# Kernel tuning notes

Measured on AMD Instinct MI355X. Metric: run time of the kernel, lower is better.

The kernel has to match this reference:

```python
import jax, jax.numpy as jnp
import numpy as np

N, D, H, E = 8192, 1024, 4096, 8


def setup_inputs() -> dict:
    key = jax.random.key(0)
    ks = jax.random.split(key, 7)
    s_d = 1.0 / np.sqrt(D)
    s_h = 1.0 / np.sqrt(H)
    return {
        "x": jax.random.normal(ks[0], (N, D), dtype=jnp.float32),
        "gate_w": jax.random.uniform(ks[1], (E, D), jnp.float32, -s_d, s_d),
        "gate_b": jax.random.uniform(ks[2], (E,), jnp.float32, -s_d, s_d),
        "w1": jax.random.uniform(ks[3], (E, D, H), jnp.float32, -s_d, s_d),
        "b1": jax.random.uniform(ks[4], (E, H), jnp.float32, -s_d, s_d),
        "w2": jax.random.uniform(ks[5], (E, H, D), jnp.float32, -s_h, s_h),
        "b2": jax.random.uniform(ks[6], (E, D), jnp.float32, -s_h, s_h),
    }


def reference(x, gate_w, gate_b, w1, b1, w2, b2):
    # gate softmax over experts: [N, E]
    gates = jax.nn.softmax(x @ gate_w.T + gate_b, axis=-1)
    # all experts in one batched GEMM pair
    h = jax.nn.relu(jnp.einsum("nd,edh->neh", x, w1) + b1)      # [N, E, H]
    expert_out = jnp.einsum("neh,ehd->ned", h, w2) + b2          # [N, E, D]
    # gated weighted sum over experts
    return jnp.einsum("ne,ned->nd", gates, expert_out)
```

## Files before the change

### kernel.cpp

```cpp
#include <hip/hip_runtime.h>
#include <hip/hip_bf16.h>

typedef _Float16 half8 __attribute__((ext_vector_type(8)));
typedef float floatx4 __attribute__((ext_vector_type(4)));

__device__ inline void gload_lds16(const void* g, void* l) {
  __builtin_amdgcn_global_load_lds(
      (const __attribute__((address_space(1))) unsigned int*)g,
      (__attribute__((address_space(3))) unsigned int*)l, 16, 0, 0);
}

__device__ inline unsigned lds_off(const void* p) {
  return (unsigned)(uintptr_t)(const __attribute__((address_space(3))) char*)p;
}
__device__ inline half8 ds_read128(unsigned off) {
  half8 r;
  asm volatile("ds_read_b128 %0, %1" : "=v"(r) : "v"(off));
  return r;
}

#define BARB()   __builtin_amdgcn_s_barrier()
#define WAITL0() asm volatile("s_waitcnt lgkmcnt(0)")
#define WAITV(n) asm volatile("s_waitcnt vmcnt(" #n ")")
#define SCHED0() __builtin_amdgcn_sched_barrier(0)

__device__ inline void xcd_chunk_decode(int* mb, int* nk) {
  const int gx = gridDim.x;
  const int nb = gx * gridDim.y;
  const int b = blockIdx.x + gx * blockIdx.y;
  const int s = (b & 7) * (nb >> 3) + (b >> 3);
  const int PW = gx * 8;
  const int p = s / PW, r = s % PW;
  *mb = r >> 3;
  *nk = p * 8 + (r & 7);
}

__global__ __launch_bounds__(256) void gates_kernel(
    const float* __restrict__ x, const float* __restrict__ gw,
    const float* __restrict__ gb, float* __restrict__ gates) {
  const int lane = threadIdx.x & 63, wid = threadIdx.x >> 6;
  const int n = blockIdx.x * 4 + wid;
  const float* xr = x + (size_t)n * 1024;
  float xv[16];
#pragma unroll
  for (int i = 0; i < 16; ++i) xv[i] = xr[lane + i * 64];
  float logit[8];
#pragma unroll
  for (int e = 0; e < 8; ++e) {
    const float* wr = gw + (size_t)e * 1024;
    float p = 0.f;
#pragma unroll
    for (int i = 0; i < 16; ++i) p += xv[i] * wr[lane + i * 64];
#pragma unroll
    for (int off = 32; off > 0; off >>= 1) p += __shfl_xor(p, off);
    logit[e] = p + gb[e];
  }
  float mx = logit[0];
#pragma unroll
  for (int e = 1; e < 8; ++e) mx = fmaxf(mx, logit[e]);
  float s = 0.f;
#pragma unroll
  for (int e = 0; e < 8; ++e) { logit[e] = expf(logit[e] - mx); s += logit[e]; }
  if (lane < 8) gates[(size_t)n * 8 + lane] = logit[lane] / s;
}

__global__ __launch_bounds__(256) void bias_init_kernel(
    const float* __restrict__ gates, const float* __restrict__ b2,
    float* __restrict__ out) {
  const int idx = blockIdx.x * 256 + threadIdx.x;
  const int n = idx >> 8;
  const int d = (idx & 255) << 2;
  const float* g = gates + (size_t)n * 8;
  floatx4 acc = {0.f, 0.f, 0.f, 0.f};
#pragma unroll
  for (int e = 0; e < 8; ++e) {
    const float ge = g[e];
    const floatx4 b = *(const floatx4*)(b2 + (size_t)e * 1024 + d);
#pragma unroll
    for (int j = 0; j < 4; ++j) acc[j] += ge * b[j];
  }
  *(floatx4*)(out + (size_t)n * 1024 + d) = acc;
}

__global__ __launch_bounds__(256) void cvt_f32_f16_kernel(
    const float* __restrict__ in, _Float16* __restrict__ out, int n8) {
  const int i = blockIdx.x * 256 + threadIdx.x;
  if (i >= n8) return;
  const float4* p = (const float4*)(in + (size_t)i * 8);
  float4 a = p[0], b = p[1];
  half8 h;
  h[0] = (_Float16)a.x; h[1] = (_Float16)a.y; h[2] = (_Float16)a.z; h[3] = (_Float16)a.w;
  h[4] = (_Float16)b.x; h[5] = (_Float16)b.y; h[6] = (_Float16)b.z; h[7] = (_Float16)b.w;
  *(half8*)(out + (size_t)i * 8) = h;
}

__global__ __launch_bounds__(256) void transpose_cvt_kernel(
    const float* __restrict__ in, _Float16* __restrict__ out, int R, int C) {
  __shared__ _Float16 tile[32][33];
  const float* src = in + (size_t)blockIdx.z * R * C;
  _Float16* dst = out + (size_t)blockIdx.z * R * C;
  const int tx = threadIdx.x & 31, ty = threadIdx.x >> 5;
  const int c0 = blockIdx.x << 5, r0 = blockIdx.y << 5;
#pragma unroll
  for (int i = 0; i < 4; ++i)
    tile[ty + i * 8][tx] = (_Float16)src[(size_t)(r0 + ty + i * 8) * C + c0 + tx];
  __syncthreads();
#pragma unroll
  for (int i = 0; i < 4; ++i)
    dst[(size_t)(c0 + ty + i * 8) * R + r0 + tx] = tile[tx][ty + i * 8];
}

__global__ __launch_bounds__(512, 2) void gemm1_kernel(
    const _Float16* __restrict__ A, const _Float16* __restrict__ Bt,
    const float* __restrict__ bias, const float* __restrict__ gates, int e,
    _Float16* __restrict__ Hout, int lda, int ldb, int K, int Nout) {
  __shared__ _Float16 smem[2][4][8192];
  const int tid = threadIdx.x, lane = tid & 63, wid = tid >> 6;
  const int wm = wid >> 2, wn = wid & 3;

  int mb, nk;
  xcd_chunk_decode(&mb, &nk);
  const int m0 = mb * 256, n0 = nk * 256;
  const int NT = K >> 6;

  floatx4 acc[8][4] = {};

  auto stage_half = [&](int h) {
    if (h >= 4 * NT) return;
    const int th = h >> 2, j = h & 3, bf = th & 1;
    const int k0 = th * 64;
    const char* gb; int ld, rorig;
    if (j < 2) { gb = (const char*)A;  ld = lda; rorig = m0 + j * 128; }
    else       { gb = (const char*)Bt; ld = ldb; rorig = n0 + (j - 2) * 128; }
    _Float16* lb = &smem[bf][j][0];
#pragma unroll
    for (int i = 0; i < 2; ++i) {
      const int row = (wid * 2 + i) * 8 + (lane >> 3);
      const int gkb = ((lane & 7) * 16) ^ ((row & 7) << 4);
      gload_lds16(gb + ((size_t)(rorig + row) * ld + k0) * 2 + gkb,
                  lb + (wid * 2 + i) * 512 + lane * 8);
    }
  };

  const unsigned smem0 = lds_off(&smem[0][0][0]);
  auto ldA = [&](int bf, int mf, int ks) -> half8 {
    const int row = mf * 16 + (lane & 15);
    const int col = (ks * 64 + ((lane >> 4) << 4)) ^ ((row & 7) << 4);
    return ds_read128(smem0 + (bf * 4 + wm) * 16384 + row * 128 + col);
  };
  auto ldB = [&](int bf, int nf, int ks) -> half8 {
    const int c = wn * 64 + nf * 16 + (lane & 15);
    const int r = c & 127;
    const int col = (ks * 64 + ((lane >> 4) << 4)) ^ ((r & 7) << 4);
    return ds_read128(smem0 + (bf * 4 + 2 + (c >> 7)) * 16384 + r * 128 + col);
  };

  stage_half(0); stage_half(1); stage_half(2); stage_half(3);
  stage_half(4 * 1 + 2); stage_half(4 * 1 + 3);
  WAITV(4); SCHED0();
  BARB();

#pragma unroll 1
  for (int t = 0; t < NT; ++t) {
    const int bf = t & 1;
    half8 a[4][2], bh[2][2], bl[2][2];
#pragma unroll
    for (int ks = 0; ks < 2; ++ks) {
#pragma unroll
      for (int m = 0; m < 4; ++m) a[m][ks] = ldA(bf, m, ks);
#pragma unroll
      for (int n = 0; n < 2; ++n) bh[n][ks] = ldB(bf, 2 + n, ks);
    }
    stage_half(4 * (t + 1) + 0);
    BARB(); WAITL0(); SCHED0();
    __builtin_amdgcn_s_setprio(1);
#pragma unroll
    for (int m = 0; m < 4; ++m)
#pragma unroll
      for (int n = 0; n < 2; ++n)
#pragma unroll
        for (int ks = 0; ks < 2; ++ks)
          acc[m][2 + n] = __builtin_amdgcn_mfma_f32_16x16x32_f16(
              a[m][ks], bh[n][ks], acc[m][2 + n], 0, 0, 0);
    __builtin_amdgcn_s_setprio(0);
    BARB();
#pragma unroll
    for (int ks = 0; ks < 2; ++ks)
#pragma unroll
      for (int n = 0; n < 2; ++n) bl[n][ks] = ldB(bf, n, ks);
    stage_half(4 * (t + 1) + 1);
    BARB(); WAITL0(); SCHED0();
    __builtin_amdgcn_s_setprio(1);
#pragma unroll
    for (int m = 0; m < 4; ++m)
#pragma unroll
      for (int n = 0; n < 2; ++n)
#pragma unroll
        for (int ks = 0; ks < 2; ++ks)
          acc[m][n] = __builtin_amdgcn_mfma_f32_16x16x32_f16(
              a[m][ks], bl[n][ks], acc[m][n], 0, 0, 0);
    __builtin_amdgcn_s_setprio(0);
    BARB();
#pragma unroll
    for (int ks = 0; ks < 2; ++ks)
#pragma unroll
      for (int m = 0; m < 4; ++m) a[m][ks] = ldA(bf, 4 + m, ks);
    stage_half(4 * (t + 2) + 2);
    BARB(); WAITL0(); SCHED0();
    __builtin_amdgcn_s_setprio(1);
#pragma unroll
    for (int m = 0; m < 4; ++m)
#pragma unroll
      for (int n = 0; n < 2; ++n)
#pragma unroll
        for (int ks = 0; ks < 2; ++ks)
          acc[4 + m][2 + n] = __builtin_amdgcn_mfma_f32_16x16x32_f16(
              a[m][ks], bh[n][ks], acc[4 + m][2 + n], 0, 0, 0);
    __builtin_amdgcn_s_setprio(0);
    BARB();
    stage_half(4 * (t + 2) + 3);
    BARB();
    __builtin_amdgcn_s_setprio(1);
#pragma unroll
    for (int m = 0; m < 4; ++m)
#pragma unroll
      for (int n = 0; n < 2; ++n)
#pragma unroll
        for (int ks = 0; ks < 2; ++ks)
          acc[4 + m][n] = __builtin_amdgcn_mfma_f32_16x16x32_f16(
              a[m][ks], bl[n][ks], acc[4 + m][n], 0, 0, 0);
    __builtin_amdgcn_s_setprio(0);
    if (t + 2 < NT) { WAITV(4); } else { WAITV(0); }
    SCHED0();
    BARB();
  }

#pragma unroll
  for (int mf = 0; mf < 8; ++mf) {
    const int gr0 = m0 + wm * 128 + mf * 16 + ((lane >> 4) << 2);
#pragma unroll
    for (int r = 0; r < 4; ++r) {
      const float g = gates[(size_t)(gr0 + r) * 8 + e];
#pragma unroll
      for (int nf = 0; nf < 4; ++nf) {
        const int gc = n0 + wn * 64 + nf * 16 + (lane & 15);
        const float v = acc[mf][nf][r] + bias[gc];
        Hout[(size_t)(gr0 + r) * Nout + gc] = (_Float16)(g * fmaxf(v, 0.0f));
      }
    }
  }
}

__global__ __launch_bounds__(512, 2) void gemm2_kernel(
    const _Float16* __restrict__ A, const _Float16* __restrict__ Bt,
    float* __restrict__ Out, int lda, int ldb, int K, int Nout) {
  __shared__ _Float16 smem[3][3][8192];
  const int tid = threadIdx.x, lane = tid & 63, wid = tid >> 6;
  const int wm = wid >> 2, wn = wid & 3;

  int mb, nk;
  xcd_chunk_decode(&mb, &nk);
  const int m0 = mb * 256, n0 = nk * 128;
  const int NT = K >> 6;

  floatx4 acc[8][2] = {};

  auto stage_half = [&](int tile, int j) {
    if (tile >= NT) return;
    const int bf = tile % 3;
    const int k0 = tile * 64;
    const char* gb; int ld, rorig;
    if (j < 2) { gb = (const char*)A;  ld = lda; rorig = m0 + j * 128; }
    else       { gb = (const char*)Bt; ld = ldb; rorig = n0; }
    _Float16* lb = &smem[bf][j][0];
#pragma unroll
    for (int i = 0; i < 2; ++i) {
      const int row = (wid * 2 + i) * 8 + (lane >> 3);
      const int gkb = ((lane & 7) * 16) ^ ((row & 7) << 4);
      gload_lds16(gb + ((size_t)(rorig + row) * ld + k0) * 2 + gkb,
                  lb + (wid * 2 + i) * 512 + lane * 8);
    }
  };

  const unsigned smem0 = lds_off(&smem[0][0][0]);
  auto ldA = [&](int bf, int mf, int ks) -> half8 {
    const int row = mf * 16 + (lane & 15);
    const int col = (ks * 64 + ((lane >> 4) << 4)) ^ ((row & 7) << 4);
    return ds_read128(smem0 + (bf * 3 + wm) * 16384 + row * 128 + col);
  };
  auto ldB = [&](int bf, int nf, int ks) -> half8 {
    const int r = wn * 32 + nf * 16 + (lane & 15);
    const int col = (ks * 64 + ((lane >> 4) << 4)) ^ ((r & 7) << 4);
    return ds_read128(smem0 + (bf * 3 + 2) * 16384 + r * 128 + col);
  };

  stage_half(0, 0); stage_half(0, 1); stage_half(0, 2);
  stage_half(1, 0); stage_half(1, 1); stage_half(1, 2);
  WAITV(6); SCHED0();
  BARB();

#pragma unroll 1
  for (int t = 0; t < NT; ++t) {
    const int bf = t % 3;
    half8 a[4][2], bb[2][2];
#pragma unroll
    for (int ks = 0; ks < 2; ++ks) {
#pragma unroll
      for (int m = 0; m < 4; ++m) a[m][ks] = ldA(bf, m, ks);
#pragma unroll
      for (int n = 0; n < 2; ++n) bb[n][ks] = ldB(bf, n, ks);
    }
    stage_half(t + 2, 0); stage_half(t + 2, 1);
    BARB(); WAITL0(); SCHED0();
    __builtin_amdgcn_s_setprio(1);
#pragma unroll
    for (int m = 0; m < 4; ++m)
#pragma unroll
      for (int n = 0; n < 2; ++n)
#pragma unroll
        for (int ks = 0; ks < 2; ++ks)
          acc[m][n] = __builtin_amdgcn_mfma_f32_16x16x32_f16(
              a[m][ks], bb[n][ks], acc[m][n], 0, 0, 0);
    __builtin_amdgcn_s_setprio(0);
    BARB();
#pragma unroll
    for (int ks = 0; ks < 2; ++ks)
#pragma unroll
      for (int m = 0; m < 4; ++m) a[m][ks] = ldA(bf, 4 + m, ks);
    stage_half(t + 2, 2);
    BARB(); WAITL0(); SCHED0();
    __builtin_amdgcn_s_setprio(1);
#pragma unroll
    for (int m = 0; m < 4; ++m)
#pragma unroll
      for (int n = 0; n < 2; ++n)
#pragma unroll
        for (int ks = 0; ks < 2; ++ks)
          acc[4 + m][n] = __builtin_amdgcn_mfma_f32_16x16x32_f16(
              a[m][ks], bb[n][ks], acc[4 + m][n], 0, 0, 0);
    __builtin_amdgcn_s_setprio(0);
    if (t + 2 < NT) { WAITV(6); } else { WAITV(0); }
    SCHED0();
    BARB();
  }

#pragma unroll
  for (int mf = 0; mf < 8; ++mf) {
    const int gr0 = m0 + wm * 128 + mf * 16 + ((lane >> 4) << 2);
#pragma unroll
    for (int nf = 0; nf < 2; ++nf) {
      const int gc = n0 + wn * 32 + nf * 16 + (lane & 15);
#pragma unroll
      for (int r = 0; r < 4; ++r) {
        float* p = Out + (size_t)(gr0 + r) * Nout + gc;
        *p = *p + acc[mf][nf][r];
      }
    }
  }
}

extern "C" void kernel_launch(void* const* d_in, const int* in_sizes, int n_in,
                              void* d_out, int out_size, void* d_ws,
                              size_t ws_size, hipStream_t stream) {
  const float* x  = (const float*)d_in[0];
  const float* gw = (const float*)d_in[1];
  const float* gb = (const float*)d_in[2];
  const float* w1 = (const float*)d_in[3];
  const float* b1 = (const float*)d_in[4];
  const float* w2 = (const float*)d_in[5];
  const float* b2 = (const float*)d_in[6];
  float* out = (float*)d_out;

  const int N = 8192, D = 1024, H = 4096, E = 8;
  const size_t MB = 1ull << 20;

  char* ws = (char*)d_ws;
  float* gates  = (float*)ws;
  _Float16* x_h = (_Float16*)(ws + MB);

  gates_kernel<<<N / 4, 256, 0, stream>>>(x, gw, gb, gates);
  bias_init_kernel<<<N * D / 4 / 256, 256, 0, stream>>>(gates, b2, out);
  cvt_f32_f16_kernel<<<(N * D / 8 + 255) / 256, 256, 0, stream>>>(x, x_h, N * D / 8);

  if (ws_size >= 210 * MB) {
    _Float16* Hbuf = (_Float16*)(ws + 17 * MB);
    _Float16* w1t  = (_Float16*)(ws + 81 * MB);
    _Float16* w2t  = (_Float16*)(ws + 145 * MB);
    transpose_cvt_kernel<<<dim3(H / 32, D / 32, E), 256, 0, stream>>>(w1, w1t, D, H);
    transpose_cvt_kernel<<<dim3(D / 32, H / 32, E), 256, 0, stream>>>(w2, w2t, H, D);
    for (int e = 0; e < E; ++e) {
      gemm1_kernel<<<dim3(N / 256, H / 256), 512, 0, stream>>>(
          x_h, w1t + (size_t)e * H * D, b1 + (size_t)e * H, gates, e, Hbuf,
          D, D, D, H);
      gemm2_kernel<<<dim3(N / 256, D / 128), 512, 0, stream>>>(
          Hbuf, w2t + (size_t)e * D * H, out, H, H, H, D);
    }
  } else {
    _Float16* w1t  = (_Float16*)(ws + 17 * MB);
    _Float16* w2t  = (_Float16*)(ws + 25 * MB);
    _Float16* Hbuf = (_Float16*)(ws + 33 * MB);
    for (int e = 0; e < E; ++e) {
      transpose_cvt_kernel<<<dim3(H / 32, D / 32, 1), 256, 0, stream>>>(
          w1 + (size_t)e * D * H, w1t, D, H);
      transpose_cvt_kernel<<<dim3(D / 32, H / 32, 1), 256, 0, stream>>>(
          w2 + (size_t)e * H * D, w2t, H, D);
      gemm1_kernel<<<dim3(N / 256, H / 256), 512, 0, stream>>>(
          x_h, w1t, b1 + (size_t)e * H, gates, e, Hbuf, D, D, D, H);
      gemm2_kernel<<<dim3(N / 256, D / 128), 512, 0, stream>>>(
          Hbuf, w2t, out, H, H, H, D);
    }
  }
}
```

Measured before the change: 1.379 ms.

## Use 256x256 split-K tile for second GEMM with separate partial buffers

The second GEMM now reuses the 256x256-tile kernel template in place of the 256x128 one. K is split in two halves, and each half accumulates into its own fp32 buffer (partial or out), so the two halves never write the same location. A final combine kernel adds the partials and the gated b2 bias, replacing the up-front bias init. The w1 transpose now runs per expert into a small buffer, which lowers the workspace requirement but puts a transpose kernel inside the loop.

```diff
diff --git a/kernel.cpp b/kernel.cpp
--- a/kernel.cpp
+++ b/kernel.cpp
@@ -9,7 +9,6 @@
       (const __attribute__((address_space(1))) unsigned int*)g,
       (__attribute__((address_space(3))) unsigned int*)l, 16, 0, 0);
 }
-
 __device__ inline unsigned lds_off(const void* p) {
   return (unsigned)(uintptr_t)(const __attribute__((address_space(3))) char*)p;
 }
@@ -18,7 +17,6 @@
   asm volatile("ds_read_b128 %0, %1" : "=v"(r) : "v"(off));
   return r;
 }
-
 #define BARB()   __builtin_amdgcn_s_barrier()
 #define WAITL0() asm volatile("s_waitcnt lgkmcnt(0)")
 #define WAITV(n) asm volatile("s_waitcnt vmcnt(" #n ")")
@@ -72,6 +70,27 @@
   const int d = (idx & 255) << 2;
   const float* g = gates + (size_t)n * 8;
   floatx4 acc = {0.f, 0.f, 0.f, 0.f};
+#pragma unroll
+  for (int e = 0; e < 8; ++e) {
+    const float ge = g[e];
+    const floatx4 b = *(const floatx4*)(b2 + (size_t)e * 1024 + d);
+#pragma unroll
+    for (int j = 0; j < 4; ++j) acc[j] += ge * b[j];
+  }
+  *(floatx4*)(out + (size_t)n * 1024 + d) = acc;
+}
+
+__global__ __launch_bounds__(256) void combine_kernel(
+    const float* __restrict__ gates, const float* __restrict__ b2,
+    const float* __restrict__ partial, float* __restrict__ out) {
+  const int idx = blockIdx.x * 256 + threadIdx.x;
+  const int n = idx >> 8;
+  const int d = (idx & 255) << 2;
+  const float* g = gates + (size_t)n * 8;
+  floatx4 acc = *(const floatx4*)(partial + (size_t)n * 1024 + d);
+  const floatx4 o = *(const floatx4*)(out + (size_t)n * 1024 + d);
+#pragma unroll
+  for (int j = 0; j < 4; ++j) acc[j] += o[j];
 #pragma unroll
   for (int e = 0; e < 8; ++e) {
     const float ge = g[e];
@@ -110,25 +129,30 @@
     dst[(size_t)(c0 + ty + i * 8) * R + r0 + tx] = tile[tx][ty + i * 8];
 }
 
-__global__ __launch_bounds__(512, 2) void gemm1_kernel(
+template <int EPI>
+__global__ __launch_bounds__(512, 2) void gemm256_kernel(
     const _Float16* __restrict__ A, const _Float16* __restrict__ Bt,
     const float* __restrict__ bias, const float* __restrict__ gates, int e,
-    _Float16* __restrict__ Hout, int lda, int ldb, int K, int Nout) {
+    _Float16* __restrict__ Hout, float* __restrict__ partial,
+    float* __restrict__ outp, int beta, int lda, int ldb, int kLen, int Nout) {
   __shared__ _Float16 smem[2][4][8192];
   const int tid = threadIdx.x, lane = tid & 63, wid = tid >> 6;
   const int wm = wid >> 2, wn = wid & 3;
 
   int mb, nk;
   xcd_chunk_decode(&mb, &nk);
-  const int m0 = mb * 256, n0 = nk * 256;
-  const int NT = K >> 6;
+  const int m0 = mb * 256;
+  int n0, kb;
+  if (EPI == 1) { n0 = (nk & 3) * 256; kb = (nk >> 2) * kLen; }
+  else          { n0 = nk * 256;       kb = 0; }
+  const int NT = kLen >> 6;
 
   floatx4 acc[8][4] = {};
 
   auto stage_half = [&](int h) {
     if (h >= 4 * NT) return;
     const int th = h >> 2, j = h & 3, bf = th & 1;
-    const int k0 = th * 64;
+    const int k0 = kb + th * 64;
     const char* gb; int ld, rorig;
     if (j < 2) { gb = (const char*)A;  ld = lda; rorig = m0 + j * 128; }
     else       { gb = (const char*)Bt; ld = ldb; rorig = n0 + (j - 2) * 128; }
@@ -240,12 +264,21 @@
     const int gr0 = m0 + wm * 128 + mf * 16 + ((lane >> 4) << 2);
 #pragma unroll
     for (int r = 0; r < 4; ++r) {
-      const float g = gates[(size_t)(gr0 + r) * 8 + e];
+      const int gr = gr0 + r;
+      float g = 0.f;
+      if (EPI == 0) g = gates[(size_t)gr * 8 + e];
 #pragma unroll
       for (int nf = 0; nf < 4; ++nf) {
         const int gc = n0 + wn * 64 + nf * 16 + (lane & 15);
-        const float v = acc[mf][nf][r] + bias[gc];
-        Hout[(size_t)(gr0 + r) * Nout + gc] = (_Float16)(g * fmaxf(v, 0.0f));
+        if (EPI == 0) {
+          const float v = acc[mf][nf][r] + bias[gc];
+          Hout[(size_t)gr * Nout + gc] = (_Float16)(g * fmaxf(v, 0.0f));
+        } else {
+          float* P = (nk >> 2) ? outp : partial;
+          float* p = P + (size_t)gr * Nout + gc;
+          if (beta) *p = *p + acc[mf][nf][r];
+          else      *p = acc[mf][nf][r];
+        }
       }
     }
   }
@@ -257,14 +290,11 @@
   __shared__ _Float16 smem[3][3][8192];
   const int tid = threadIdx.x, lane = tid & 63, wid = tid >> 6;
   const int wm = wid >> 2, wn = wid & 3;
-
   int mb, nk;
   xcd_chunk_decode(&mb, &nk);
   const int m0 = mb * 256, n0 = nk * 128;
   const int NT = K >> 6;
-
   floatx4 acc[8][2] = {};
-
   auto stage_half = [&](int tile, int j) {
     if (tile >= NT) return;
     const int bf = tile % 3;
@@ -281,7 +311,6 @@
                   lb + (wid * 2 + i) * 512 + lane * 8);
     }
   };
-
   const unsigned smem0 = lds_off(&smem[0][0][0]);
   auto ldA = [&](int bf, int mf, int ks) -> half8 {
     const int row = mf * 16 + (lane & 15);
@@ -293,12 +322,10 @@
     const int col = (ks * 64 + ((lane >> 4) << 4)) ^ ((r & 7) << 4);
     return ds_read128(smem0 + (bf * 3 + 2) * 16384 + r * 128 + col);
   };
-
   stage_half(0, 0); stage_half(0, 1); stage_half(0, 2);
   stage_half(1, 0); stage_half(1, 1); stage_half(1, 2);
   WAITV(6); SCHED0();
   BARB();
-
 #pragma unroll 1
   for (int t = 0; t < NT; ++t) {
     const int bf = t % 3;
@@ -343,7 +370,6 @@
     SCHED0();
     BARB();
   }
-
 #pragma unroll
   for (int mf = 0; mf < 8; ++mf) {
     const int gr0 = m0 + wm * 128 + mf * 16 + ((lane >> 4) << 2);
@@ -379,33 +405,38 @@
   _Float16* x_h = (_Float16*)(ws + MB);
 
   gates_kernel<<<N / 4, 256, 0, stream>>>(x, gw, gb, gates);
-  bias_init_kernel<<<N * D / 4 / 256, 256, 0, stream>>>(gates, b2, out);
   cvt_f32_f16_kernel<<<(N * D / 8 + 255) / 256, 256, 0, stream>>>(x, x_h, N * D / 8);
 
-  if (ws_size >= 210 * MB) {
-    _Float16* Hbuf = (_Float16*)(ws + 17 * MB);
-    _Float16* w1t  = (_Float16*)(ws + 81 * MB);
-    _Float16* w2t  = (_Float16*)(ws + 145 * MB);
-    transpose_cvt_kernel<<<dim3(H / 32, D / 32, E), 256, 0, stream>>>(w1, w1t, D, H);
+  if (ws_size >= 186 * MB) {
+    _Float16* Hbuf   = (_Float16*)(ws + 17 * MB);
+    _Float16* w2t    = (_Float16*)(ws + 81 * MB);
+    _Float16* w1t    = (_Float16*)(ws + 145 * MB);
+    float*    partial = (float*)(ws + 153 * MB);
     transpose_cvt_kernel<<<dim3(D / 32, H / 32, E), 256, 0, stream>>>(w2, w2t, H, D);
     for (int e = 0; e < E; ++e) {
-      gemm1_kernel<<<dim3(N / 256, H / 256), 512, 0, stream>>>(
-          x_h, w1t + (size_t)e * H * D, b1 + (size_t)e * H, gates, e, Hbuf,
+      transpose_cvt_kernel<<<dim3(H / 32, D / 32, 1), 256, 0, stream>>>(
+          w1 + (size_t)e * D * H, w1t, D, H);
+      gemm256_kernel<0><<<dim3(N / 256, H / 256), 512, 0, stream>>>(
+          x_h, w1t, b1 + (size_t)e * H, gates, e, Hbuf, nullptr, nullptr, 0,
           D, D, D, H);
-      gemm2_kernel<<<dim3(N / 256, D / 128), 512, 0, stream>>>(
-          Hbuf, w2t + (size_t)e * D * H, out, H, H, H, D);
-    }
+      gemm256_kernel<1><<<dim3(N / 256, 8), 512, 0, stream>>>(
+          Hbuf, w2t + (size_t)e * D * H, nullptr, nullptr, e, nullptr,
+          partial, out, e > 0, H, H, H / 2, D);
+    }
+    combine_kernel<<<N * D / 4 / 256, 256, 0, stream>>>(gates, b2, partial, out);
   } else {
     _Float16* w1t  = (_Float16*)(ws + 17 * MB);
     _Float16* w2t  = (_Float16*)(ws + 25 * MB);
     _Float16* Hbuf = (_Float16*)(ws + 33 * MB);
+    bias_init_kernel<<<N * D / 4 / 256, 256, 0, stream>>>(gates, b2, out);
     for (int e = 0; e < E; ++e) {
       transpose_cvt_kernel<<<dim3(H / 32, D / 32, 1), 256, 0, stream>>>(
           w1 + (size_t)e * D * H, w1t, D, H);
       transpose_cvt_kernel<<<dim3(D / 32, H / 32, 1), 256, 0, stream>>>(
           w2 + (size_t)e * H * D, w2t, H, D);
-      gemm1_kernel<<<dim3(N / 256, H / 256), 512, 0, stream>>>(
-          x_h, w1t, b1 + (size_t)e * H, gates, e, Hbuf, D, D, D, H);
+      gemm256_kernel<0><<<dim3(N / 256, H / 256), 512, 0, stream>>>(
+          x_h, w1t, b1 + (size_t)e * H, gates, e, Hbuf, nullptr, nullptr, 0,
+          D, D, D, H);
       gemm2_kernel<<<dim3(N / 256, D / 128), 512, 0, stream>>>(
           Hbuf, w2t, out, H, H, H, D);
     }
```

Measured after the change: 1.348 ms. 2.2% less time.

## Replace gemm2 with split-K 128x128 kernel and fold bias into a combine pass

Applied to the files above, without the earlier changes.

The tuned 256x128 triple-buffered gemm2 is replaced by a simpler 128x128-tile kernel that splits K in two across blockIdx.z. That quadruples the block count to fill more CUs. Each K-half accumulates into its own fp32 buffer (a partial workspace or the output). A final combine kernel adds the two halves plus the gated b2 bias, replacing the up-front bias init. The new kernel drops the LDS swizzle, the priority hints and the deeper pipelining, so LDS bank conflicts and exposed load latency may offset the gain in parallelism. The smallest-workspace fallback has both K-halves doing read-modify-write into the same output, which races.

```diff
diff --git a/kernel.cpp b/kernel.cpp
--- a/kernel.cpp
+++ b/kernel.cpp
@@ -9,7 +9,6 @@
       (const __attribute__((address_space(1))) unsigned int*)g,
       (__attribute__((address_space(3))) unsigned int*)l, 16, 0, 0);
 }
-
 __device__ inline unsigned lds_off(const void* p) {
   return (unsigned)(uintptr_t)(const __attribute__((address_space(3))) char*)p;
 }
@@ -18,7 +17,6 @@
   asm volatile("ds_read_b128 %0, %1" : "=v"(r) : "v"(off));
   return r;
 }
-
 #define BARB()   __builtin_amdgcn_s_barrier()
 #define WAITL0() asm volatile("s_waitcnt lgkmcnt(0)")
 #define WAITV(n) asm volatile("s_waitcnt vmcnt(" #n ")")
@@ -72,6 +70,27 @@
   const int d = (idx & 255) << 2;
   const float* g = gates + (size_t)n * 8;
   floatx4 acc = {0.f, 0.f, 0.f, 0.f};
+#pragma unroll
+  for (int e = 0; e < 8; ++e) {
+    const float ge = g[e];
+    const floatx4 b = *(const floatx4*)(b2 + (size_t)e * 1024 + d);
+#pragma unroll
+    for (int j = 0; j < 4; ++j) acc[j] += ge * b[j];
+  }
+  *(floatx4*)(out + (size_t)n * 1024 + d) = acc;
+}
+
+__global__ __launch_bounds__(256) void combine_kernel(
+    const float* __restrict__ gates, const float* __restrict__ b2,
+    const float* __restrict__ partial, float* __restrict__ out) {
+  const int idx = blockIdx.x * 256 + threadIdx.x;
+  const int n = idx >> 8;
+  const int d = (idx & 255) << 2;
+  const float* g = gates + (size_t)n * 8;
+  floatx4 acc = *(const floatx4*)(partial + (size_t)n * 1024 + d);
+  const floatx4 o = *(const floatx4*)(out + (size_t)n * 1024 + d);
+#pragma unroll
+  for (int j = 0; j < 4; ++j) acc[j] += o[j];
 #pragma unroll
   for (int e = 0; e < 8; ++e) {
     const float ge = g[e];
@@ -113,7 +132,7 @@
 __global__ __launch_bounds__(512, 2) void gemm1_kernel(
     const _Float16* __restrict__ A, const _Float16* __restrict__ Bt,
     const float* __restrict__ bias, const float* __restrict__ gates, int e,
-    _Float16* __restrict__ Hout, int lda, int ldb, int K, int Nout) {
+    _Float16* __restrict__ Hout, int lda, int ldb, int kLen, int Nout) {
   __shared__ _Float16 smem[2][4][8192];
   const int tid = threadIdx.x, lane = tid & 63, wid = tid >> 6;
   const int wm = wid >> 2, wn = wid & 3;
@@ -121,7 +140,7 @@
   int mb, nk;
   xcd_chunk_decode(&mb, &nk);
   const int m0 = mb * 256, n0 = nk * 256;
-  const int NT = K >> 6;
+  const int NT = kLen >> 6;
 
   floatx4 acc[8][4] = {};
 
@@ -251,109 +270,71 @@
   }
 }
 
-__global__ __launch_bounds__(512, 2) void gemm2_kernel(
+__global__ __launch_bounds__(256, 2) void gemm2_128_kernel(
     const _Float16* __restrict__ A, const _Float16* __restrict__ Bt,
-    float* __restrict__ Out, int lda, int ldb, int K, int Nout) {
-  __shared__ _Float16 smem[3][3][8192];
+    float* __restrict__ partial, float* __restrict__ outp, int beta,
+    int lda, int ldb, int kLen, int Nout) {
+  __shared__ _Float16 As[2][128 * 32];
+  __shared__ _Float16 Bs[2][128 * 32];
   const int tid = threadIdx.x, lane = tid & 63, wid = tid >> 6;
-  const int wm = wid >> 2, wn = wid & 3;
-
-  int mb, nk;
-  xcd_chunk_decode(&mb, &nk);
-  const int m0 = mb * 256, n0 = nk * 128;
-  const int NT = K >> 6;
-
-  floatx4 acc[8][2] = {};
-
-  auto stage_half = [&](int tile, int j) {
-    if (tile >= NT) return;
-    const int bf = tile % 3;
-    const int k0 = tile * 64;
-    const char* gb; int ld, rorig;
-    if (j < 2) { gb = (const char*)A;  ld = lda; rorig = m0 + j * 128; }
-    else       { gb = (const char*)Bt; ld = ldb; rorig = n0; }
-    _Float16* lb = &smem[bf][j][0];
-#pragma unroll
-    for (int i = 0; i < 2; ++i) {
-      const int row = (wid * 2 + i) * 8 + (lane >> 3);
-      const int gkb = ((lane & 7) * 16) ^ ((row & 7) << 4);
-      gload_lds16(gb + ((size_t)(rorig + row) * ld + k0) * 2 + gkb,
-                  lb + (wid * 2 + i) * 512 + lane * 8);
+  const int wr = wid >> 1, wc = wid & 1;
+  const int m0 = blockIdx.x * 128, n0 = blockIdx.y * 128;
+  const int kb = blockIdx.z * kLen;
+
+  floatx4 acc[4][4] = {};
+
+  auto stage = [&](int buf, int kt) {
+    const int k0 = kb + (kt << 5);
+#pragma unroll
+    for (int it = 0; it < 2; ++it) {
+      const int s = tid + it * 256;
+      gload_lds16(A + (size_t)(m0 + (s >> 2)) * lda + k0 + (s & 3) * 8,
+                  &As[buf][s * 8]);
+    }
+#pragma unroll
+    for (int it = 0; it < 2; ++it) {
+      const int s = tid + it * 256;
+      gload_lds16(Bt + (size_t)(n0 + (s >> 2)) * ldb + k0 + (s & 3) * 8,
+                  &Bs[buf][s * 8]);
     }
   };
 
-  const unsigned smem0 = lds_off(&smem[0][0][0]);
-  auto ldA = [&](int bf, int mf, int ks) -> half8 {
-    const int row = mf * 16 + (lane & 15);
-    const int col = (ks * 64 + ((lane >> 4) << 4)) ^ ((row & 7) << 4);
-    return ds_read128(smem0 + (bf * 3 + wm) * 16384 + row * 128 + col);
-  };
-  auto ldB = [&](int bf, int nf, int ks) -> half8 {
-    const int r = wn * 32 + nf * 16 + (lane & 15);
-    const int col = (ks * 64 + ((lane >> 4) << 4)) ^ ((r & 7) << 4);
-    return ds_read128(smem0 + (bf * 3 + 2) * 16384 + r * 128 + col);
-  };
-
-  stage_half(0, 0); stage_half(0, 1); stage_half(0, 2);
-  stage_half(1, 0); stage_half(1, 1); stage_half(1, 2);
-  WAITV(6); SCHED0();
-  BARB();
-
-#pragma unroll 1
-  for (int t = 0; t < NT; ++t) {
-    const int bf = t % 3;
-    half8 a[4][2], bb[2][2];
-#pragma unroll
-    for (int ks = 0; ks < 2; ++ks) {
-#pragma unroll
-      for (int m = 0; m < 4; ++m) a[m][ks] = ldA(bf, m, ks);
-#pragma unroll
-      for (int n = 0; n < 2; ++n) bb[n][ks] = ldB(bf, n, ks);
-    }
-    stage_half(t + 2, 0); stage_half(t + 2, 1);
-    BARB(); WAITL0(); SCHED0();
-    __builtin_amdgcn_s_setprio(1);
-#pragma unroll
-    for (int m = 0; m < 4; ++m)
-#pragma unroll
-      for (int n = 0; n < 2; ++n)
-#pragma unroll
-        for (int ks = 0; ks < 2; ++ks)
-          acc[m][n] = __builtin_amdgcn_mfma_f32_16x16x32_f16(
-              a[m][ks], bb[n][ks], acc[m][n], 0, 0, 0);
-    __builtin_amdgcn_s_setprio(0);
-    BARB();
-#pragma unroll
-    for (int ks = 0; ks < 2; ++ks)
-#pragma unroll
-      for (int m = 0; m < 4; ++m) a[m][ks] = ldA(bf, 4 + m, ks);
-    stage_half(t + 2, 2);
-    BARB(); WAITL0(); SCHED0();
-    __builtin_amdgcn_s_setprio(1);
-#pragma unroll
-    for (int m = 0; m < 4; ++m)
-#pragma unroll
-      for (int n = 0; n < 2; ++n)
-#pragma unroll
-        for (int ks = 0; ks < 2; ++ks)
-          acc[4 + m][n] = __builtin_amdgcn_mfma_f32_16x16x32_f16(
-              a[m][ks], bb[n][ks], acc[4 + m][n], 0, 0, 0);
-    __builtin_amdgcn_s_setprio(0);
-    if (t + 2 < NT) { WAITV(6); } else { WAITV(0); }
-    SCHED0();
-    BARB();
-  }
-
-#pragma unroll
-  for (int mf = 0; mf < 8; ++mf) {
-    const int gr0 = m0 + wm * 128 + mf * 16 + ((lane >> 4) << 2);
-#pragma unroll
-    for (int nf = 0; nf < 2; ++nf) {
-      const int gc = n0 + wn * 32 + nf * 16 + (lane & 15);
+  const int nk = kLen >> 5;
+  stage(0, 0);
+  __syncthreads();
+
+  for (int kt = 0; kt < nk; ++kt) {
+    const int cur = kt & 1;
+    if (kt + 1 < nk) stage(cur ^ 1, kt + 1);
+    const int krow = (lane >> 4) * 8;
+    half8 af[4], bfr[4];
+#pragma unroll
+    for (int m = 0; m < 4; ++m)
+      af[m] = *(const half8*)&As[cur][(wr * 64 + m * 16 + (lane & 15)) * 32 + krow];
+#pragma unroll
+    for (int n = 0; n < 4; ++n)
+      bfr[n] = *(const half8*)&Bs[cur][(wc * 64 + n * 16 + (lane & 15)) * 32 + krow];
+#pragma unroll
+    for (int m = 0; m < 4; ++m)
+#pragma unroll
+      for (int n = 0; n < 4; ++n)
+        acc[m][n] =
+            __builtin_amdgcn_mfma_f32_16x16x32_f16(af[m], bfr[n], acc[m][n], 0, 0, 0);
+    __syncthreads();
+  }
+
+  float* P = blockIdx.z ? outp : partial;
+#pragma unroll
+  for (int m = 0; m < 4; ++m) {
+    const int gr0 = m0 + wr * 64 + m * 16 + ((lane >> 4) << 2);
+#pragma unroll
+    for (int n = 0; n < 4; ++n) {
+      const int gc = n0 + wc * 64 + n * 16 + (lane & 15);
 #pragma unroll
       for (int r = 0; r < 4; ++r) {
-        float* p = Out + (size_t)(gr0 + r) * Nout + gc;
-        *p = *p + acc[mf][nf][r];
+        float* p = P + (size_t)(gr0 + r) * Nout + gc;
+        if (beta) *p = *p + acc[m][n][r];
+        else      *p = acc[m][n][r];
       }
     }
   }
@@ -379,26 +360,44 @@
   _Float16* x_h = (_Float16*)(ws + MB);
 
   gates_kernel<<<N / 4, 256, 0, stream>>>(x, gw, gb, gates);
-  bias_init_kernel<<<N * D / 4 / 256, 256, 0, stream>>>(gates, b2, out);
   cvt_f32_f16_kernel<<<(N * D / 8 + 255) / 256, 256, 0, stream>>>(x, x_h, N * D / 8);
 
-  if (ws_size >= 210 * MB) {
-    _Float16* Hbuf = (_Float16*)(ws + 17 * MB);
-    _Float16* w1t  = (_Float16*)(ws + 81 * MB);
-    _Float16* w2t  = (_Float16*)(ws + 145 * MB);
+  if (ws_size >= 242 * MB) {
+    _Float16* Hbuf    = (_Float16*)(ws + 17 * MB);
+    _Float16* w2t     = (_Float16*)(ws + 81 * MB);
+    _Float16* w1t     = (_Float16*)(ws + 145 * MB);
+    float*    partial = (float*)(ws + 209 * MB);
+    transpose_cvt_kernel<<<dim3(D / 32, H / 32, E), 256, 0, stream>>>(w2, w2t, H, D);
     transpose_cvt_kernel<<<dim3(H / 32, D / 32, E), 256, 0, stream>>>(w1, w1t, D, H);
-    transpose_cvt_kernel<<<dim3(D / 32, H / 32, E), 256, 0, stream>>>(w2, w2t, H, D);
     for (int e = 0; e < E; ++e) {
       gemm1_kernel<<<dim3(N / 256, H / 256), 512, 0, stream>>>(
           x_h, w1t + (size_t)e * H * D, b1 + (size_t)e * H, gates, e, Hbuf,
           D, D, D, H);
-      gemm2_kernel<<<dim3(N / 256, D / 128), 512, 0, stream>>>(
-          Hbuf, w2t + (size_t)e * D * H, out, H, H, H, D);
-    }
+      gemm2_128_kernel<<<dim3(N / 128, D / 128, 2), 256, 0, stream>>>(
+          Hbuf, w2t + (size_t)e * D * H, partial, out, e > 0, H, H, H / 2, D);
+    }
+    combine_kernel<<<N * D / 4 / 256, 256, 0, stream>>>(gates, b2, partial, out);
+  } else if (ws_size >= 186 * MB) {
+    _Float16* Hbuf    = (_Float16*)(ws + 17 * MB);
+    _Float16* w2t     = (_Float16*)(ws + 81 * MB);
+    _Float16* w1t     = (_Float16*)(ws + 145 * MB);
+    float*    partial = (float*)(ws + 153 * MB);
+    transpose_cvt_kernel<<<dim3(D / 32, H / 32, E), 256, 0, stream>>>(w2, w2t, H, D);
+    for (int e = 0; e < E; ++e) {
+      transpose_cvt_kernel<<<dim3(H / 32, D / 32, 1), 256, 0, stream>>>(
+          w1 + (size_t)e * D * H, w1t, D, H);
+      gemm1_kernel<<<dim3(N / 256, H / 256), 512, 0, stream>>>(
+          x_h, w1t, b1 + (size_t)e * H, gates, e, Hbuf, D, D, D, H);
+      gemm2_128_kernel<<<dim3(N / 128, D / 128, 2), 256, 0, stream>>>(
+          Hbuf, w2t + (size_t)e * D * H, partial, out, e > 0, H, H, H / 2, D);
+    }
+    combine_kernel<<<N * D / 4 / 256, 256, 0, stream>>>(gates, b2, partial, out);
   } else {
     _Float16* w1t  = (_Float16*)(ws + 17 * MB);
     _Float16* w2t  = (_Float16*)(ws + 25 * MB);
     _Float16* Hbuf = (_Float16*)(ws + 33 * MB);
+    float* partial = (float*)(ws + 97 * MB);
+    bias_init_kernel<<<N * D / 4 / 256, 256, 0, stream>>>(gates, b2, out);
     for (int e = 0; e < E; ++e) {
       transpose_cvt_kernel<<<dim3(H / 32, D / 32, 1), 256, 0, stream>>>(
           w1 + (size_t)e * D * H, w1t, D, H);
@@ -406,8 +405,8 @@
           w2 + (size_t)e * H * D, w2t, H, D);
       gemm1_kernel<<<dim3(N / 256, H / 256), 512, 0, stream>>>(
           x_h, w1t, b1 + (size_t)e * H, gates, e, Hbuf, D, D, D, H);
-      gemm2_kernel<<<dim3(N / 256, D / 128), 512, 0, stream>>>(
-          Hbuf, w2t, out, H, H, H, D);
-    }
-  }
-}
+      gemm2_128_kernel<<<dim3(N / 128, D / 128, 2), 256, 0, stream>>>(
+          Hbuf, w2t, out, out, 1, H, H, H / 2, D);
+    }
+  }
+}
```

Measured after the change: 1.482 ms. +7.5%, slower.
